# Optimization experiments

Hardware: AMD Instinct MI355X
Metric: run time of the kernel (lower is better)

The kernel has to match this reference:

```python
import jax, jax.numpy as jnp
import numpy as np


def _bilinear_sample(fea, gx, gy):
    """grid_sample, bilinear, zero padding, align_corners=True.
    fea: [B,C,H,W]; gx, gy: [B,N] normalized coords in [-1,1]. Returns [B,N,C]."""
    B, C, H, W = fea.shape
    feaT = fea.transpose(0, 2, 3, 1)  # [B,H,W,C]
    x = (gx + 1.0) * ((W - 1) * 0.5)
    y = (gy + 1.0) * ((H - 1) * 0.5)
    x0 = jnp.floor(x)
    y0 = jnp.floor(y)
    bidx = jnp.arange(B)[:, None]
    out = jnp.zeros(gx.shape + (C,), fea.dtype)
    for dx, dy in ((0, 0), (1, 0), (0, 1), (1, 1)):
        xi = x0 + dx
        yi = y0 + dy
        w = (1.0 - jnp.abs(x - xi)) * (1.0 - jnp.abs(y - yi))
        valid = (xi >= 0) & (xi <= W - 1) & (yi >= 0) & (yi <= H - 1)
        xic = jnp.clip(xi, 0, W - 1).astype(jnp.int32)
        yic = jnp.clip(yi, 0, H - 1).astype(jnp.int32)
        vals = feaT[bidx, yic, xic]  # [B,N,C]
        out = out + (w * valid.astype(fea.dtype))[:, :, None] * vals
    return out


def _homo_warping(src_fea, src_proj, ref_proj, depth_values):
    """src_fea [B,C,H,W]; src_proj/ref_proj [B,4,4]; depth_values [B,D,H,W].
    Returns warped volume [B,C,D,H,W]."""
    B, C, H, W = src_fea.shape
    D = depth_values.shape[1]
    proj = jnp.einsum('bij,bjk->bik', src_proj, jnp.linalg.inv(ref_proj))
    rot = proj[:, :3, :3]
    trans = proj[:, :3, 3]
    ys, xs = jnp.meshgrid(jnp.arange(H, dtype=src_fea.dtype),
                          jnp.arange(W, dtype=src_fea.dtype), indexing='ij')
    xyz = jnp.stack([xs.ravel(), ys.ravel(), jnp.ones(H * W, src_fea.dtype)], 0)  # [3,HW]
    rot_xyz = jnp.einsum('bij,jn->bin', rot, xyz)  # [B,3,HW]
    d = depth_values.reshape(B, 1, D, H * W)
    pxyz = rot_xyz[:, :, None, :] * d + trans[:, :, None, None]  # [B,3,D,HW]
    z = pxyz[:, 2]
    gx = pxyz[:, 0] / z
    gy = pxyz[:, 1] / z
    nx = gx / ((W - 1) * 0.5) - 1.0
    ny = gy / ((H - 1) * 0.5) - 1.0
    sampled = _bilinear_sample(src_fea, nx.reshape(B, -1), ny.reshape(B, -1))  # [B,D*H*W,C]
    return sampled.reshape(B, D, H, W, C).transpose(0, 4, 1, 2, 3)


def _combine_proj(proj):
    """proj [B,2,4,4]: [:,0]=extrinsic 4x4, [:,1,:3,:3]=intrinsic. Returns [B,4,4]."""
    upd = jnp.einsum('bij,bjk->bik', proj[:, 1, :3, :3], proj[:, 0, :3, :4])
    return proj[:, 0].at[:, :3, :4].set(upd)


def setup_inputs() -> dict:
    B, V, C, H, W, D = 2, 5, 32, 256, 320, 4
    key = jax.random.key(0)
    feats = jax.random.normal(key, (B, V, C, H, W), dtype=jnp.float32)
    rng = np.random.default_rng(0)
    K = np.eye(4, dtype=np.float32)
    K[0, 0] = 0.9 * W; K[1, 1] = 0.9 * W; K[0, 2] = W / 2.0; K[1, 2] = H / 2.0
    projs = np.zeros((B, V, 2, 4, 4), dtype=np.float32)
    for b in range(B):
        for v in range(V):
            ang = 0.0 if v == 0 else float(rng.uniform(-0.05, 0.05))
            ca, sa = np.cos(ang), np.sin(ang)
            E = np.eye(4, dtype=np.float32)
            E[:3, :3] = np.array([[ca, 0, sa], [0, 1, 0], [-sa, 0, ca]], dtype=np.float32)
            if v > 0:
                E[:3, 3] = rng.uniform(-20, 20, size=3).astype(np.float32)
            projs[b, v, 0] = E
            projs[b, v, 1] = K
    dmin, dmax = 425.0, 935.0
    base = np.linspace(dmin, dmax, D, dtype=np.float32)
    depth = np.broadcast_to(base[None, :, None, None], (B, D, H, W)).copy()
    depth += rng.uniform(-5, 5, size=(B, D, H, W)).astype(np.float32)
    return {'feats': feats,
            'proj_matrices': jnp.asarray(projs),
            'depth_values': jnp.asarray(depth)}


def reference(feats, proj_matrices, depth_values):
    """HAMMER.get_volume_variance_and_mask.
    feats [B,V,C,H,W], proj_matrices [B,V,2,4,4], depth_values [B,D,H,W].
    Returns (volume_variance [B,C,D,H,W], cv_mask [B,H,W])."""
    B, V, C, H, W = feats.shape
    D = depth_values.shape[1]
    ref_proj = _combine_proj(proj_matrices[:, 0])
    ref_vol = jnp.broadcast_to(feats[:, 0, :, None], (B, C, D, H, W))
    vol_sum = ref_vol
    vol_sq = ref_vol ** 2
    cv_mask = jnp.zeros((B, H, W), feats.dtype)
    for v in range(1, V):
        src_proj = _combine_proj(proj_matrices[:, v])
        warped = _homo_warping(feats[:, v], src_proj, ref_proj, depth_values)
        cv_mask = cv_mask + jnp.count_nonzero(
            jnp.count_nonzero(warped, axis=1), axis=1).astype(feats.dtype)
        vol_sum = vol_sum + warped
        vol_sq = vol_sq + warped ** 2
    inv_v = 1.0 / V
    volume_variance = vol_sq * inv_v - (vol_sum * inv_v) ** 2
    return volume_variance, cv_mask
```

## Files before the change

### kernel.cpp

```cpp
#include <hip/hip_runtime.h>

constexpr int B = 2, V = 5, C = 32, H = 256, W = 320, D = 4;
constexpr int HW = H * W;

__device__ float g_rt[B * (V - 1) * 12];

__device__ void combine_np(const float* __restrict__ proj, int b, int v, float Mo[4][4]) {
    const float* E = proj + ((size_t)(b * V + v) * 2 + 0) * 16;
    const float* K = proj + ((size_t)(b * V + v) * 2 + 1) * 16;
    for (int i = 0; i < 3; i++)
        for (int j = 0; j < 4; j++) {
            float acc = __fadd_rn(0.0f, __fmul_rn(K[i * 4 + 0], E[0 * 4 + j]));
            acc = __fadd_rn(acc, __fmul_rn(K[i * 4 + 1], E[1 * 4 + j]));
            acc = __fadd_rn(acc, __fmul_rn(K[i * 4 + 2], E[2 * 4 + j]));
            Mo[i][j] = acc;
        }
    for (int j = 0; j < 4; j++) Mo[3][j] = E[3 * 4 + j];
}

__global__ void setup_proj(const float* __restrict__ proj) {
    int t = threadIdx.x;
    if (t >= B * (V - 1)) return;
    int b = t / (V - 1);
    int v = t % (V - 1) + 1;

    float R[4][4], S[4][4];
    combine_np(proj, b, 0, R);
    combine_np(proj, b, v, S);

    float I4[4][4];
    for (int i = 0; i < 4; i++)
        for (int j = 0; j < 4; j++) I4[i][j] = 0.0f;

    float d0 = __fdiv_rn(1.0f, R[0][0]);
    I4[0][0] = d0;
    float d1 = __fdiv_rn(1.0f, R[1][1]);
    I4[1][1] = d1;
    {
        float x0 = R[0][1];
        if (x0 != 0.0f) x0 = __fmul_rn(x0, I4[0][0]);
        I4[0][1] = __fmul_rn(x0, -d1);
    }
    float d2 = __fdiv_rn(1.0f, R[2][2]);
    I4[2][2] = d2;
    {
        float x0 = R[0][2], x1 = R[1][2];
        if (x0 != 0.0f) x0 = __fmul_rn(x0, I4[0][0]);
        if (x1 != 0.0f) {
            x0 = __fadd_rn(x0, __fmul_rn(x1, I4[0][1]));
            x1 = __fmul_rn(x1, I4[1][1]);
        }
        I4[0][2] = __fmul_rn(x0, -d2);
        I4[1][2] = __fmul_rn(x1, -d2);
    }
    float d3 = __fdiv_rn(1.0f, R[3][3]);
    I4[3][3] = d3;
    {
        float x0 = R[0][3], x1 = R[1][3], x2 = R[2][3];
        if (x0 != 0.0f) x0 = __fmul_rn(x0, I4[0][0]);
        if (x1 != 0.0f) {
            x0 = __fadd_rn(x0, __fmul_rn(x1, I4[0][1]));
            x1 = __fmul_rn(x1, I4[1][1]);
        }
        if (x2 != 0.0f) {
            x0 = __fadd_rn(x0, __fmul_rn(x2, I4[0][2]));
            x1 = __fadd_rn(x1, __fmul_rn(x2, I4[1][2]));
            x2 = __fmul_rn(x2, I4[2][2]);
        }
        I4[0][3] = __fmul_rn(x0, -d3);
        I4[1][3] = __fmul_rn(x1, -d3);
        I4[2][3] = __fmul_rn(x2, -d3);
    }

    float P[3][4];
    for (int i = 0; i < 3; i++)
        for (int k = 0; k < 4; k++) {
            float acc = 0.0f;
            for (int j = 0; j < 4; j++)
                acc = __fadd_rn(acc, __fmul_rn(S[i][j], I4[j][k]));
            P[i][k] = acc;
        }

    float* out = g_rt + t * 12;
    out[0] = P[0][0]; out[1] = P[0][1]; out[2] = P[0][2];
    out[3] = P[1][0]; out[4] = P[1][1]; out[5] = P[1][2];
    out[6] = P[2][0]; out[7] = P[2][1]; out[8] = P[2][2];
    out[9] = P[0][3]; out[10] = P[1][3]; out[11] = P[2][3];
}

__global__ __launch_bounds__(256) void warp_var(
    const float* __restrict__ feats,
    const float* __restrict__ depthv,
    float* __restrict__ var_out,
    float* __restrict__ mask_out)
{
    int idx = blockIdx.x * 256 + threadIdx.x;
    int w = idx % W;
    int h = (idx / W) % H;
    int d = (idx / HW) % D;
    int b = idx / (HW * D);

    float depth = depthv[idx];

    const float* refF = feats + (size_t)b * V * C * HW + (size_t)h * W + w;
    float sum[C], sq[C];
#pragma unroll
    for (int c = 0; c < C; c++) {
        float rv = refF[(size_t)c * HW];
        sum[c] = rv;
        sq[c] = rv * rv;
    }

    float maskc = 0.0f;
    const float xf = (float)w, yf = (float)h;
    const float hwX = 0.5f * (float)(W - 1);
    const float hwY = 0.5f * (float)(H - 1);
    const float rcpX = 1.0f / 159.5f;
    const float rcpY = 1.0f / 127.5f;

    for (int v = 1; v < V; v++) {
        const float* P = g_rt + ((size_t)b * (V - 1) + (v - 1)) * 12;
        float rx = __fadd_rn(__fmaf_rn(P[1], yf, __fmul_rn(P[0], xf)), P[2]);
        float ry = __fadd_rn(__fmaf_rn(P[4], yf, __fmul_rn(P[3], xf)), P[5]);
        float rz = __fadd_rn(__fmaf_rn(P[7], yf, __fmul_rn(P[6], xf)), P[8]);
        float px = __fadd_rn(__fmul_rn(rx, depth), P[9]);
        float py = __fadd_rn(__fmul_rn(ry, depth), P[10]);
        float pz = __fadd_rn(__fmul_rn(rz, depth), P[11]);
        float gx = __fdiv_rn(px, pz);
        float gy = __fdiv_rn(py, pz);
        float nx = __fadd_rn(__fmul_rn(gx, rcpX), -1.0f);
        float ny = __fadd_rn(__fmul_rn(gy, rcpY), -1.0f);
        float x = __fmul_rn(__fadd_rn(nx, 1.0f), hwX);
        float y = __fmul_rn(__fadd_rn(ny, 1.0f), hwY);

        float x0 = floorf(x), y0 = floorf(y);
        float x1 = x0 + 1.0f, y1 = y0 + 1.0f;

        float wx0 = __fadd_rn(1.0f, -fabsf(__fadd_rn(x, -x0)));
        float wx1 = __fadd_rn(1.0f, -fabsf(__fadd_rn(x, -x1)));
        float wy0 = __fadd_rn(1.0f, -fabsf(__fadd_rn(y, -y0)));
        float wy1 = __fadd_rn(1.0f, -fabsf(__fadd_rn(y, -y1)));

        float vx0 = (x0 >= 0.0f && x0 <= (float)(W - 1)) ? 1.0f : 0.0f;
        float vx1 = (x1 >= 0.0f && x1 <= (float)(W - 1)) ? 1.0f : 0.0f;
        float vy0 = (y0 >= 0.0f && y0 <= (float)(H - 1)) ? 1.0f : 0.0f;
        float vy1 = (y1 >= 0.0f && y1 <= (float)(H - 1)) ? 1.0f : 0.0f;

        float s00 = __fmul_rn(__fmul_rn(wx0, wy0), __fmul_rn(vx0, vy0));
        float s10 = __fmul_rn(__fmul_rn(wx1, wy0), __fmul_rn(vx1, vy0));
        float s01 = __fmul_rn(__fmul_rn(wx0, wy1), __fmul_rn(vx0, vy1));
        float s11 = __fmul_rn(__fmul_rn(wx1, wy1), __fmul_rn(vx1, vy1));

        int xi0 = (int)fminf(fmaxf(x0, 0.0f), (float)(W - 1));
        int xi1 = (int)fminf(fmaxf(x1, 0.0f), (float)(W - 1));
        int yi0 = (int)fminf(fmaxf(y0, 0.0f), (float)(H - 1));
        int yi1 = (int)fminf(fmaxf(y1, 0.0f), (float)(H - 1));
        int o00 = yi0 * W + xi0;
        int o10 = yi0 * W + xi1;
        int o01 = yi1 * W + xi0;
        int o11 = yi1 * W + xi1;

        const float* S = feats + ((size_t)(b * V + v) * C) * HW;
        bool anynz = false;
#pragma unroll
        for (int c = 0; c < C; c++) {
            const float* Sc = S + (size_t)c * HW;
            float f00 = Sc[o00];
            float f10 = Sc[o10];
            float f01 = Sc[o01];
            float f11 = Sc[o11];
            float val = s00 * f00 + s10 * f10 + s01 * f01 + s11 * f11;
            anynz = anynz || (val != 0.0f);
            sum[c] += val;
            sq[c] += val * val;
        }
        maskc += anynz ? 1.0f : 0.0f;
    }

    const float inv_v = 1.0f / (float)V;
    size_t obase = ((size_t)b * C * D + d) * HW + (size_t)h * W + w;
#pragma unroll
    for (int c = 0; c < C; c++) {
        float s = sum[c] * inv_v;
        float vv = sq[c] * inv_v - s * s;
        var_out[obase + (size_t)c * D * HW] = vv;
    }

    atomicAdd(&mask_out[(size_t)b * HW + (size_t)h * W + w], maskc);
}

extern "C" void kernel_launch(void* const* d_in, const int* in_sizes, int n_in,
                              void* d_out, int out_size, void* d_ws, size_t ws_size,
                              hipStream_t stream) {
    const float* feats = (const float*)d_in[0];
    const float* proj = (const float*)d_in[1];
    const float* depthv = (const float*)d_in[2];

    float* var = (float*)d_out;
    float* mask = var + (size_t)B * C * D * HW;

    hipMemsetAsync(mask, 0, sizeof(float) * (size_t)B * HW, stream);

    setup_proj<<<1, 64, 0, stream>>>(proj);

    int n = B * D * HW;
    warp_var<<<n / 256, 256, 0, stream>>>(feats, depthv, var, mask);
}
```

Before: 274.9 us.

## Interchange view/channel loops to drop per-channel accumulators and stream outputs

Precomputes the bilinear offsets and weights for all four source views up front, then loops over channels with views innermost. Each channel's variance is finished and written immediately instead of keeping 64 sum/square registers live, which lowers register pressure and should raise occupancy. Output stores become nontemporal, and the mask count is tracked as a bitmask. In exchange it keeps 32 offsets and weights live, and the gathers are ordered channel-major.

```diff
diff --git a/kernel.cpp b/kernel.cpp
--- a/kernel.cpp
+++ b/kernel.cpp
@@ -102,22 +102,16 @@
 
     float depth = depthv[idx];
 
-    const float* refF = feats + (size_t)b * V * C * HW + (size_t)h * W + w;
-    float sum[C], sq[C];
-#pragma unroll
-    for (int c = 0; c < C; c++) {
-        float rv = refF[(size_t)c * HW];
-        sum[c] = rv;
-        sq[c] = rv * rv;
-    }
-
-    float maskc = 0.0f;
     const float xf = (float)w, yf = (float)h;
     const float hwX = 0.5f * (float)(W - 1);
     const float hwY = 0.5f * (float)(H - 1);
     const float rcpX = 1.0f / 159.5f;
     const float rcpY = 1.0f / 127.5f;
 
+    int   toff[V - 1][4];
+    float twt[V - 1][4];
+
+#pragma unroll
     for (int v = 1; v < V; v++) {
         const float* P = g_rt + ((size_t)b * (V - 1) + (v - 1)) * 12;
         float rx = __fadd_rn(__fmaf_rn(P[1], yf, __fmul_rn(P[0], xf)), P[2]);
@@ -155,37 +149,47 @@
         int xi1 = (int)fminf(fmaxf(x1, 0.0f), (float)(W - 1));
         int yi0 = (int)fminf(fmaxf(y0, 0.0f), (float)(H - 1));
         int yi1 = (int)fminf(fmaxf(y1, 0.0f), (float)(H - 1));
-        int o00 = yi0 * W + xi0;
-        int o10 = yi0 * W + xi1;
-        int o01 = yi1 * W + xi0;
-        int o11 = yi1 * W + xi1;
-
-        const float* S = feats + ((size_t)(b * V + v) * C) * HW;
-        bool anynz = false;
+
+        int vb = (b * V + v) * C * HW;
+        toff[v - 1][0] = vb + yi0 * W + xi0;
+        toff[v - 1][1] = vb + yi0 * W + xi1;
+        toff[v - 1][2] = vb + yi1 * W + xi0;
+        toff[v - 1][3] = vb + yi1 * W + xi1;
+        twt[v - 1][0] = s00;
+        twt[v - 1][1] = s10;
+        twt[v - 1][2] = s01;
+        twt[v - 1][3] = s11;
+    }
+
+    const int rb = b * V * C * HW + h * W + w;
+    const float inv_v = 1.0f / (float)V;
+    const size_t obase = ((size_t)b * C * D + d) * HW + (size_t)h * W + w;
+
+    int nzmask = 0;
+
+#pragma unroll 2
+    for (int c = 0; c < C; c++) {
+        const int cofs = c * HW;
+        float rv = feats[rb + cofs];
+        float s = rv;
+        float q = rv * rv;
 #pragma unroll
-        for (int c = 0; c < C; c++) {
-            const float* Sc = S + (size_t)c * HW;
-            float f00 = Sc[o00];
-            float f10 = Sc[o10];
-            float f01 = Sc[o01];
-            float f11 = Sc[o11];
-            float val = s00 * f00 + s10 * f10 + s01 * f01 + s11 * f11;
-            anynz = anynz || (val != 0.0f);
-            sum[c] += val;
-            sq[c] += val * val;
-        }
-        maskc += anynz ? 1.0f : 0.0f;
-    }
-
-    const float inv_v = 1.0f / (float)V;
-    size_t obase = ((size_t)b * C * D + d) * HW + (size_t)h * W + w;
-#pragma unroll
-    for (int c = 0; c < C; c++) {
-        float s = sum[c] * inv_v;
-        float vv = sq[c] * inv_v - s * s;
-        var_out[obase + (size_t)c * D * HW] = vv;
-    }
-
+        for (int v = 0; v < V - 1; v++) {
+            float f00 = feats[toff[v][0] + cofs];
+            float f10 = feats[toff[v][1] + cofs];
+            float f01 = feats[toff[v][2] + cofs];
+            float f11 = feats[toff[v][3] + cofs];
+            float val = twt[v][0] * f00 + twt[v][1] * f10 + twt[v][2] * f01 + twt[v][3] * f11;
+            nzmask |= (val != 0.0f) ? (1 << v) : 0;
+            s += val;
+            q += val * val;
+        }
+        float sm = s * inv_v;
+        float vv = q * inv_v - sm * sm;
+        __builtin_nontemporal_store(vv, &var_out[obase + (size_t)c * (D * HW)]);
+    }
+
+    float maskc = (float)__popc(nzmask);
     atomicAdd(&mask_out[(size_t)b * HW + (size_t)h * W + w], maskc);
 }
 
```

Result: no change. 277.7 us (+1.0%).
